# Performance work log

Hardware: AMD Instinct MI355X
Metric: run time of the kernel (lower is better)

## Reference

```python
import jax, jax.numpy as jnp
import numpy as np


def setup_inputs() -> dict:
    key = jax.random.key(0)
    ks = jax.random.split(key, 4)
    B, T, D, H = 64, 512, 512, 1024
    return {
        "x": jax.random.normal(ks[0], (B, T, D), dtype=jnp.float32),
        "kz": jax.random.normal(ks[1], (D, H), dtype=jnp.float32) * (1.0 / np.sqrt(D)),
        "kr": jax.random.normal(ks[2], (D, H), dtype=jnp.float32) * (1.0 / np.sqrt(D)),
        "kh": jax.random.normal(ks[3], (D, H), dtype=jnp.float32) * (1.0 / np.sqrt(D)),
        "mz": jnp.ones((H,), dtype=jnp.float32),
        "mr": jnp.ones((H,), dtype=jnp.float32),
        "br": jnp.zeros((H,), dtype=jnp.float32),
        "bz": jnp.zeros((H,), dtype=jnp.float32),
    }


def reference(x, kz, kr, kh, mz, mr, br, bz):
    B, T, D = x.shape
    H = kz.shape[1]
    # Precompute input projections for all timesteps (batched GEMMs),
    # identical math to per-step matmuls in the original cell.
    xz = jnp.einsum("btd,dh->bth", x, kz)  # [B,T,H]
    xr = jnp.einsum("btd,dh->bth", x, kr)
    xh = jnp.einsum("btd,dh->bth", x, kh)

    def step(h, inp):
        xz_t, xr_t, xh_t = inp  # each [B,H]
        r = jnp.tanh(xr_t + h * mr + br) + 1.0
        z = jax.nn.sigmoid(xz_t + h * mz + bz)
        h_new = z * h + (1.0 - z) * jnp.tanh(xh_t + r * h)
        return h_new, h_new

    h0 = jnp.zeros((B, H), dtype=x.dtype)
    # scan over time axis: move T to leading dim
    xs = (jnp.swapaxes(xz, 0, 1), jnp.swapaxes(xr, 0, 1), jnp.swapaxes(xh, 0, 1))
    _, ys = jax.lax.scan(step, h0, xs)  # ys: [T,B,H]
    return jnp.swapaxes(ys, 0, 1)  # [B,T,H]
```

## Files before the change

kernel.cpp:

```cpp
#include <hip/hip_runtime.h>
#include <hip/hip_bf16.h>
#include <math.h>


#define M_DIM 32768
#define K_DIM 512
#define H_DIM 1024
#define N3    3072

typedef _Float16 half8v __attribute__((ext_vector_type(8)));
typedef _Float16 half4v __attribute__((ext_vector_type(4)));
typedef float f32x4 __attribute__((ext_vector_type(4)));

__device__ __forceinline__ f32x4 mfma16(half8v a, half8v b, f32x4 c) {
    return __builtin_amdgcn_mfma_f32_16x16x32_f16(a, b, c, 0, 0, 0);
}

__device__ __forceinline__ void load_lds16(const void* g, void* l) {
    __builtin_amdgcn_global_load_lds(
        (const __attribute__((address_space(1))) void*)g,
        (__attribute__((address_space(3))) void*)l, 16, 0, 0);
}

__global__ __launch_bounds__(256) void convert_x(
    const float4* __restrict__ x4, half4v* __restrict__ hi4,
    half4v* __restrict__ lo4, int n4)
{
    int i = blockIdx.x * 256 + threadIdx.x;
    if (i >= n4) return;
    float4 v = x4[i];
    half4v h, lo;
    h.x = (_Float16)v.x; lo.x = (_Float16)(v.x - (float)h.x);
    h.y = (_Float16)v.y; lo.y = (_Float16)(v.y - (float)h.y);
    h.z = (_Float16)v.z; lo.z = (_Float16)(v.z - (float)h.z);
    h.w = (_Float16)v.w; lo.w = (_Float16)(v.w - (float)h.w);
    hi4[i] = h; lo4[i] = lo;
}

__global__ __launch_bounds__(256) void convert_wt_t(
    const float* __restrict__ kz, const float* __restrict__ kr,
    const float* __restrict__ kh, _Float16* __restrict__ wth,
    _Float16* __restrict__ wtl)
{
    __shared__ float lds[64][65];
    const int bid = blockIdx.x;
    const int w = bid >> 7;
    const int rem = bid & 127;
    const int k0 = (rem >> 4) * 64;
    const int n0 = (rem & 15) * 64;
    const int tid = threadIdx.x;
    const float* s = (w == 0) ? kz : ((w == 1) ? kr : kh);

#pragma unroll
    for (int r = 0; r < 4; ++r) {
        const int kk = (tid >> 4) + r * 16;
        const int nn = (tid & 15) * 4;
        float4 v = *(const float4*)&s[(size_t)(k0 + kk) * H_DIM + n0 + nn];
        lds[kk][nn + 0] = v.x; lds[kk][nn + 1] = v.y;
        lds[kk][nn + 2] = v.z; lds[kk][nn + 3] = v.w;
    }
    __syncthreads();
#pragma unroll
    for (int r = 0; r < 4; ++r) {
        const int nr = (tid >> 4) + r * 16;
        const int kb = (tid & 15) * 4;
        half4v hi, lo;
#pragma unroll
        for (int i = 0; i < 4; ++i) {
            float v = lds[kb + i][nr];
            _Float16 h = (_Float16)v;
            hi[i] = h; lo[i] = (_Float16)(v - (float)h);
        }
        const size_t o = ((size_t)(w * H_DIM + n0 + nr)) * K_DIM + k0 + kb;
        *(half4v*)&wth[o] = hi;
        *(half4v*)&wtl[o] = lo;
    }
}

template<bool TR>
__global__ __launch_bounds__(256) void gemm_mfma_split(
    const _Float16* __restrict__ Ahi, const _Float16* __restrict__ Alo,
    const _Float16* __restrict__ Bthi, const _Float16* __restrict__ Btlo,
    float* __restrict__ XZ, float* __restrict__ XR, float* __restrict__ OUT)
{
    __shared__ _Float16 Ah[128 * 32];
    __shared__ _Float16 Al[128 * 32];
    __shared__ _Float16 Bh[128 * 32];
    __shared__ _Float16 Bl[128 * 32];

    const int tid = threadIdx.x;
    const int w = tid >> 6, l = tid & 63;
    const int l15 = l & 15, quad = l >> 4;
    const int bx = blockIdx.x, by = blockIdx.y;
    const long m0 = (long)by * 128;
    const long n0 = (long)bx * 128;

    f32x4 acc[4][4] = {};

    const int s1 = tid, s2 = tid + 256;
    const long aoff1 = (m0 + (s1 >> 2)) * K_DIM + (s1 & 3) * 8;
    const long aoff2 = (m0 + (s2 >> 2)) * K_DIM + (s2 & 3) * 8;
    const long boff1 = (n0 + (s1 >> 2)) * K_DIM + (s1 & 3) * 8;
    const long boff2 = (n0 + (s2 >> 2)) * K_DIM + (s2 & 3) * 8;

    const _Float16* a1 = Ahi + aoff1;  const _Float16* a2 = Ahi + aoff2;
    const _Float16* q1 = Alo + aoff1;  const _Float16* q2 = Alo + aoff2;
    const _Float16* b1 = Bthi + boff1; const _Float16* b2 = Bthi + boff2;
    const _Float16* c1 = Btlo + boff1; const _Float16* c2 = Btlo + boff2;

    _Float16* ldsA1 = &Ah[w * 512]; _Float16* ldsA2 = &Ah[2048 + w * 512];
    _Float16* ldsQ1 = &Al[w * 512]; _Float16* ldsQ2 = &Al[2048 + w * 512];
    _Float16* ldsB1 = &Bh[w * 512]; _Float16* ldsB2 = &Bh[2048 + w * 512];
    _Float16* ldsC1 = &Bl[w * 512]; _Float16* ldsC2 = &Bl[2048 + w * 512];

    const int wm = (w >> 1) * 64, wn = (w & 1) * 64;

    for (int kk = 0; kk < K_DIM / 32; ++kk) {
        load_lds16(a1, ldsA1); load_lds16(a2, ldsA2);
        load_lds16(q1, ldsQ1); load_lds16(q2, ldsQ2);
        load_lds16(b1, ldsB1); load_lds16(b2, ldsB2);
        load_lds16(c1, ldsC1); load_lds16(c2, ldsC2);
        a1 += 32; a2 += 32; q1 += 32; q2 += 32;
        b1 += 32; b2 += 32; c1 += 32; c2 += 32;
        __syncthreads();

        half8v afh[4], afl[4], bfh[4], bfl[4];
#pragma unroll
        for (int mi = 0; mi < 4; ++mi) {
            int row = (wm + mi * 16 + l15) * 32 + quad * 8;
            afh[mi] = *(const half8v*)&Ah[row];
            afl[mi] = *(const half8v*)&Al[row];
        }
#pragma unroll
        for (int ni = 0; ni < 4; ++ni) {
            int row = (wn + ni * 16 + l15) * 32 + quad * 8;
            bfh[ni] = *(const half8v*)&Bh[row];
            bfl[ni] = *(const half8v*)&Bl[row];
        }
#pragma unroll
        for (int mi = 0; mi < 4; ++mi)
#pragma unroll
            for (int ni = 0; ni < 4; ++ni) {
                acc[mi][ni] = mfma16(afh[mi], bfh[ni], acc[mi][ni]);
                acc[mi][ni] = mfma16(afh[mi], bfl[ni], acc[mi][ni]);
                acc[mi][ni] = mfma16(afl[mi], bfh[ni], acc[mi][ni]);
            }
        __syncthreads();
    }

    if (!TR) {
        float* dst = (bx < 8) ? XZ : ((bx < 16) ? XR : OUT);
        const long nl = (long)(bx & 7) * 128 + wn + l15;
#pragma unroll
        for (int mi = 0; mi < 4; ++mi) {
            const long m = m0 + wm + mi * 16 + quad * 4;
#pragma unroll
            for (int ni = 0; ni < 4; ++ni) {
                float* p = dst + m * H_DIM + nl + ni * 16;
#pragma unroll
                for (int i = 0; i < 4; ++i)
                    p[(long)i * H_DIM] = acc[mi][ni][i];
            }
        }
    } else {
        float* dst = (bx < 8) ? XZ : ((bx < 16) ? XR : OUT);
#pragma unroll
        for (int mi = 0; mi < 4; ++mi) {
            const long m = m0 + wm + mi * 16 + quad * 4;
            const long b = m >> 9;
            const long t = m & 511;
#pragma unroll
            for (int ni = 0; ni < 4; ++ni) {
                const long n = (long)(bx & 7) * 128 + wn + ni * 16 + l15;
                *(f32x4*)&dst[((size_t)(b * H_DIM + n) << 9) + t] = acc[mi][ni];
            }
        }
    }
}

#define BM 128
#define BN 128
#define BK 8
__global__ __launch_bounds__(256) void gemm_f32(
    const float* __restrict__ A, const float* __restrict__ B,
    float* __restrict__ C, int M, int N, int K)
{
    __shared__ float As[BK][BM];
    __shared__ float Bs[BK][BN];
    const int tid = threadIdx.x;
    const int bm = blockIdx.y * BM, bn = blockIdx.x * BN;
    const int tx = tid & 15, ty = tid >> 4;
    float acc[8][8];
#pragma unroll
    for (int i = 0; i < 8; i++)
#pragma unroll
        for (int j = 0; j < 8; j++) acc[i][j] = 0.f;
    const int a_row = tid >> 1, a_k = (tid & 1) * 4;
    const int b_row = tid >> 5, b_col = (tid & 31) * 4;
    const float* Aptr = A + (size_t)(bm + a_row) * K + a_k;
    const float* Bptr = B + (size_t)b_row * N + bn + b_col;
    for (int k0 = 0; k0 < K; k0 += BK) {
        float4 av = *(const float4*)(Aptr + k0);
        float4 bv = *(const float4*)(Bptr + (size_t)k0 * N);
        As[a_k + 0][a_row] = av.x; As[a_k + 1][a_row] = av.y;
        As[a_k + 2][a_row] = av.z; As[a_k + 3][a_row] = av.w;
        *(float4*)&Bs[b_row][b_col] = bv;
        __syncthreads();
#pragma unroll
        for (int kk = 0; kk < BK; kk++) {
            float4 a0 = *(const float4*)&As[kk][ty * 8];
            float4 a1 = *(const float4*)&As[kk][ty * 8 + 4];
            float4 b0 = *(const float4*)&Bs[kk][tx * 8];
            float4 b1 = *(const float4*)&Bs[kk][tx * 8 + 4];
            float a[8] = {a0.x, a0.y, a0.z, a0.w, a1.x, a1.y, a1.z, a1.w};
            float b[8] = {b0.x, b0.y, b0.z, b0.w, b1.x, b1.y, b1.z, b1.w};
#pragma unroll
            for (int i = 0; i < 8; i++)
#pragma unroll
                for (int j = 0; j < 8; j++)
                    acc[i][j] = fmaf(a[i], b[j], acc[i][j]);
        }
        __syncthreads();
    }
    float* Cptr = C + (size_t)(bm + ty * 8) * N + bn + tx * 8;
#pragma unroll
    for (int i = 0; i < 8; i++) {
        float4 c0 = {acc[i][0], acc[i][1], acc[i][2], acc[i][3]};
        float4 c1 = {acc[i][4], acc[i][5], acc[i][6], acc[i][7]};
        *(float4*)(Cptr + (size_t)i * N)     = c0;
        *(float4*)(Cptr + (size_t)i * N + 4) = c1;
    }
}

__device__ __forceinline__ float vrcp_nr(float d) {
    float r = __builtin_amdgcn_rcpf(d);
    return r * fmaf(-d, r, 2.0f);
}

__global__ __launch_bounds__(256) void scan_t(
    const float* __restrict__ XZt, const float* __restrict__ XRt,
    const float* __restrict__ XHt, float* __restrict__ out,
    const float* __restrict__ mz, const float* __restrict__ mr,
    const float* __restrict__ br, const float* __restrict__ bz)
{
    const int gid = blockIdx.x * blockDim.x + threadIdx.x;
    const int b = gid >> 10;
    const int h = gid & (H_DIM - 1);

    const float mzK = -mz[h];
    const float mrK = -2.0f * mr[h];
    const float bzK = -bz[h];
    const float brK = -2.0f * br[h];
    float hs = 0.f;

    const size_t sbase = ((size_t)(b * H_DIM + h)) << 9;
    const float4* pz = (const float4*)(XZt + sbase);
    const float4* pr = (const float4*)(XRt + sbase);
    const float4* ph = (const float4*)(XHt + sbase);
    float* const po = out + ((size_t)b << 19) + h;

    float cz[32], cr[32], ch[32];
#pragma unroll
    for (int q = 0; q < 8; ++q) {
        float4 vz = pz[q], vr = pr[q], vh = ph[q];
        cz[q*4+0] = bzK - vz.x; cz[q*4+1] = bzK - vz.y;
        cz[q*4+2] = bzK - vz.z; cz[q*4+3] = bzK - vz.w;
        cr[q*4+0] = fmaf(-2.0f, vr.x, brK); cr[q*4+1] = fmaf(-2.0f, vr.y, brK);
        cr[q*4+2] = fmaf(-2.0f, vr.z, brK); cr[q*4+3] = fmaf(-2.0f, vr.w, brK);
        ch[q*4+0] = -2.0f * vh.x; ch[q*4+1] = -2.0f * vh.y;
        ch[q*4+2] = -2.0f * vh.z; ch[q*4+3] = -2.0f * vh.w;
    }
    for (int t0 = 0; t0 < 512; t0 += 32) {
        float4 nz4[8], nr4[8], nh4[8];
        const bool more = (t0 + 32) < 512;
        if (more) {
            const int b4 = (t0 + 32) >> 2;
#pragma unroll
            for (int q = 0; q < 8; ++q) {
                nz4[q] = pz[b4 + q]; nr4[q] = pr[b4 + q]; nh4[q] = ph[b4 + q];
            }
        }
        float* pout = po + ((size_t)t0 << 10);
#pragma unroll
        for (int j = 0; j < 32; ++j) {
            const float u1   = fmaf(hs, mrK, cr[j]);
            const float uz   = fmaf(hs, mzK, cz[j]);
            const float hsK2 = -4.0f * hs;
            const float e1 = __expf(u1);
            const float s1 = vrcp_nr(e1 + 1.0f);
            const float ez = __expf(uz);
            const float sz = vrcp_nr(ez + 1.0f);
            const float u2 = fmaf(s1, hsK2, ch[j]);
            const float e2 = __expf(u2);
            const float s2 = vrcp_nr(e2 + 1.0f);
            const float th = fmaf(2.0f, s2, -1.0f);
            const float hn = fmaf(sz, hs - th, th);
            *pout = hn; pout += H_DIM;
            hs = hn;
        }
        if (more) {
#pragma unroll
            for (int q = 0; q < 8; ++q) {
                cz[q*4+0] = bzK - nz4[q].x; cz[q*4+1] = bzK - nz4[q].y;
                cz[q*4+2] = bzK - nz4[q].z; cz[q*4+3] = bzK - nz4[q].w;
                cr[q*4+0] = fmaf(-2.0f, nr4[q].x, brK);
                cr[q*4+1] = fmaf(-2.0f, nr4[q].y, brK);
                cr[q*4+2] = fmaf(-2.0f, nr4[q].z, brK);
                cr[q*4+3] = fmaf(-2.0f, nr4[q].w, brK);
                ch[q*4+0] = -2.0f * nh4[q].x; ch[q*4+1] = -2.0f * nh4[q].y;
                ch[q*4+2] = -2.0f * nh4[q].z; ch[q*4+3] = -2.0f * nh4[q].w;
            }
        }
    }
}

__global__ __launch_bounds__(256) void scan_kernel(
    const float* __restrict__ XZ, const float* __restrict__ XR,
    float* __restrict__ OUT,
    const float* __restrict__ mz, const float* __restrict__ mr,
    const float* __restrict__ br, const float* __restrict__ bz)
{
    const int gid = blockIdx.x * blockDim.x + threadIdx.x;
    const int b = gid >> 10;
    const int h = gid & (H_DIM - 1);

    const float mzK = -mz[h];
    const float mrK = -2.0f * mr[h];
    const float bzK = -bz[h];
    const float brK = -2.0f * br[h];
    float hs = 0.f;
    size_t idx = (size_t)b * 512 * H_DIM + h;

    float cz[16], cr[16], ch[16];
#pragma unroll
    for (int j = 0; j < 16; ++j) {
        cz[j] = bzK - XZ[idx + (size_t)j * H_DIM];
        cr[j] = fmaf(-2.0f, XR[idx + (size_t)j * H_DIM], brK);
        ch[j] = -2.0f * OUT[idx + (size_t)j * H_DIM];
    }
    for (int t0 = 0; t0 < 512; t0 += 16) {
        float nz[16], nr[16], nh[16];
        const bool more = (t0 + 16) < 512;
        const size_t nidx = idx + 16ul * H_DIM;
        if (more) {
#pragma unroll
            for (int j = 0; j < 16; ++j) {
                nz[j] = XZ[nidx + (size_t)j * H_DIM];
                nr[j] = XR[nidx + (size_t)j * H_DIM];
                nh[j] = OUT[nidx + (size_t)j * H_DIM];
            }
        }
#pragma unroll
        for (int j = 0; j < 16; ++j) {
            const float u1   = fmaf(hs, mrK, cr[j]);
            const float uz   = fmaf(hs, mzK, cz[j]);
            const float hsK2 = -4.0f * hs;
            const float e1 = __expf(u1);
            const float s1 = vrcp_nr(e1 + 1.0f);
            const float ez = __expf(uz);
            const float sz = vrcp_nr(ez + 1.0f);
            const float u2 = fmaf(s1, hsK2, ch[j]);
            const float e2 = __expf(u2);
            const float s2 = vrcp_nr(e2 + 1.0f);
            const float th = fmaf(2.0f, s2, -1.0f);
            const float hn = fmaf(sz, hs - th, th);
            OUT[idx + (size_t)j * H_DIM] = hn;
            hs = hn;
        }
        idx = nidx;
        if (more) {
#pragma unroll
            for (int j = 0; j < 16; ++j) {
                cz[j] = bzK - nz[j];
                cr[j] = fmaf(-2.0f, nr[j], brK);
                ch[j] = -2.0f * nh[j];
            }
        }
    }
}

extern "C" void kernel_launch(void* const* d_in, const int* in_sizes, int n_in,
                              void* d_out, int out_size, void* d_ws, size_t ws_size,
                              hipStream_t stream) {
    const float* x  = (const float*)d_in[0];
    const float* kz = (const float*)d_in[1];
    const float* kr = (const float*)d_in[2];
    const float* kh = (const float*)d_in[3];
    const float* mz = (const float*)d_in[4];
    const float* mr = (const float*)d_in[5];
    const float* br = (const float*)d_in[6];
    const float* bz = (const float*)d_in[7];
    float* out = (float*)d_out;

    char* ws = (char*)d_ws;
    const int n4 = M_DIM * K_DIM / 4;

    const size_t need_t = 476053504ul;
    const size_t need_o = 341835776ul;

    if (ws_size >= need_t) {
        float* XZt = (float*)ws;
        float* XRt = (float*)(ws + 134217728ul);
        float* XHt = (float*)(ws + 268435456ul);
        _Float16* XHI = (_Float16*)(ws + 402653184ul);
        _Float16* XLO = (_Float16*)(ws + 436207616ul);
        _Float16* WTH = (_Float16*)(ws + 469762048ul);
        _Float16* WTL = (_Float16*)(ws + 472907776ul);

        convert_x<<<n4 / 256, 256, 0, stream>>>(
            (const float4*)x, (half4v*)XHI, (half4v*)XLO, n4);
        convert_wt_t<<<384, 256, 0, stream>>>(kz, kr, kh, WTH, WTL);
        dim3 grid(N3 / 128, M_DIM / 128);
        gemm_mfma_split<true><<<grid, 256, 0, stream>>>(
            XHI, XLO, WTH, WTL, XZt, XRt, XHt);
        scan_t<<<(64 * H_DIM) / 256, 256, 0, stream>>>(
            XZt, XRt, XHt, out, mz, mr, br, bz);
    } else if (ws_size >= need_o) {
        float* XZ = (float*)ws;
        float* XR = (float*)(ws + 134217728ul);
        _Float16* XHI = (_Float16*)(ws + 268435456ul);
        _Float16* XLO = (_Float16*)(ws + 301989888ul);
        _Float16* WTH = (_Float16*)(ws + 335544320ul);
        _Float16* WTL = (_Float16*)(ws + 338690048ul);

        convert_x<<<n4 / 256, 256, 0, stream>>>(
            (const float4*)x, (half4v*)XHI, (half4v*)XLO, n4);
        convert_wt_t<<<384, 256, 0, stream>>>(kz, kr, kh, WTH, WTL);
        dim3 grid(N3 / 128, M_DIM / 128);
        gemm_mfma_split<false><<<grid, 256, 0, stream>>>(
            XHI, XLO, WTH, WTL, XZ, XR, out);
        scan_kernel<<<(64 * H_DIM) / 256, 256, 0, stream>>>(
            XZ, XR, out, mz, mr, br, bz);
    } else {
        float* XZ = (float*)ws;
        float* XR = (float*)(ws + 134217728ul);
        dim3 grid(H_DIM / BN, M_DIM / BM);
        gemm_f32<<<grid, 256, 0, stream>>>(x, kz, XZ,  M_DIM, H_DIM, K_DIM);
        gemm_f32<<<grid, 256, 0, stream>>>(x, kr, XR,  M_DIM, H_DIM, K_DIM);
        gemm_f32<<<grid, 256, 0, stream>>>(x, kh, out, M_DIM, H_DIM, K_DIM);
        scan_kernel<<<(64 * H_DIM) / 256, 256, 0, stream>>>(
            XZ, XR, out, mz, mr, br, bz);
    }
}
```

Measured before the change: 601.6 us.

## Store GEMM projections row-major with padded stride instead of transposed layout

The GEMM epilogue now writes XZ/XR/XH in [B*T, H] layout with a padded row stride of 1088 instead of the per-(b,h) time-contiguous transposed layout. The scan reads one coalesced element per thread per timestep across h, prefetching 16 steps ahead instead of 32. The padding is meant to avoid channel/bank conflicts from power-of-two strides, and the coalesced reads replace per-thread float4 loads strided by 2KB. It uses more workspace and has scalar strided reads and a shorter prefetch window.

```diff
diff --git a/kernel.cpp b/kernel.cpp
--- a/kernel.cpp
+++ b/kernel.cpp
@@ -6,6 +6,7 @@
 #define M_DIM 32768
 #define K_DIM 512
 #define H_DIM 1024
+#define HPAD  1088
 #define N3    3072
 
 typedef _Float16 half8v __attribute__((ext_vector_type(8)));
@@ -77,7 +78,7 @@
     }
 }
 
-template<bool TR>
+template<bool PAD>
 __global__ __launch_bounds__(256) void gemm_mfma_split(
     const _Float16* __restrict__ Ahi, const _Float16* __restrict__ Alo,
     const _Float16* __restrict__ Bthi, const _Float16* __restrict__ Btlo,
@@ -148,32 +149,18 @@
         __syncthreads();
     }
 
-    if (!TR) {
-        float* dst = (bx < 8) ? XZ : ((bx < 16) ? XR : OUT);
-        const long nl = (long)(bx & 7) * 128 + wn + l15;
-#pragma unroll
-        for (int mi = 0; mi < 4; ++mi) {
-            const long m = m0 + wm + mi * 16 + quad * 4;
-#pragma unroll
-            for (int ni = 0; ni < 4; ++ni) {
-                float* p = dst + m * H_DIM + nl + ni * 16;
-#pragma unroll
-                for (int i = 0; i < 4; ++i)
-                    p[(long)i * H_DIM] = acc[mi][ni][i];
-            }
-        }
-    } else {
-        float* dst = (bx < 8) ? XZ : ((bx < 16) ? XR : OUT);
-#pragma unroll
-        for (int mi = 0; mi < 4; ++mi) {
-            const long m = m0 + wm + mi * 16 + quad * 4;
-            const long b = m >> 9;
-            const long t = m & 511;
-#pragma unroll
-            for (int ni = 0; ni < 4; ++ni) {
-                const long n = (long)(bx & 7) * 128 + wn + ni * 16 + l15;
-                *(f32x4*)&dst[((size_t)(b * H_DIM + n) << 9) + t] = acc[mi][ni];
-            }
+    const long stride = PAD ? HPAD : H_DIM;
+    float* dst = (bx < 8) ? XZ : ((bx < 16) ? XR : OUT);
+    const long nl = (long)(bx & 7) * 128 + wn + l15;
+#pragma unroll
+    for (int mi = 0; mi < 4; ++mi) {
+        const long m = m0 + wm + mi * 16 + quad * 4;
+#pragma unroll
+        for (int ni = 0; ni < 4; ++ni) {
+            float* p = dst + m * stride + nl + ni * 16;
+#pragma unroll
+            for (int i = 0; i < 4; ++i)
+                p[(long)i * stride] = acc[mi][ni][i];
         }
     }
 }
@@ -237,9 +224,9 @@
     return r * fmaf(-d, r, 2.0f);
 }
 
-__global__ __launch_bounds__(256) void scan_t(
-    const float* __restrict__ XZt, const float* __restrict__ XRt,
-    const float* __restrict__ XHt, float* __restrict__ out,
+__global__ __launch_bounds__(256) void scan_pad(
+    const float* __restrict__ XZ, const float* __restrict__ XR,
+    const float* __restrict__ XH, float* __restrict__ out,
     const float* __restrict__ mz, const float* __restrict__ mr,
     const float* __restrict__ br, const float* __restrict__ bz)
 {
@@ -252,37 +239,30 @@
     const float bzK = -bz[h];
     const float brK = -2.0f * br[h];
     float hs = 0.f;
-
-    const size_t sbase = ((size_t)(b * H_DIM + h)) << 9;
-    const float4* pz = (const float4*)(XZt + sbase);
-    const float4* pr = (const float4*)(XRt + sbase);
-    const float4* ph = (const float4*)(XHt + sbase);
-    float* const po = out + ((size_t)b << 19) + h;
-
-    float cz[32], cr[32], ch[32];
-#pragma unroll
-    for (int q = 0; q < 8; ++q) {
-        float4 vz = pz[q], vr = pr[q], vh = ph[q];
-        cz[q*4+0] = bzK - vz.x; cz[q*4+1] = bzK - vz.y;
-        cz[q*4+2] = bzK - vz.z; cz[q*4+3] = bzK - vz.w;
-        cr[q*4+0] = fmaf(-2.0f, vr.x, brK); cr[q*4+1] = fmaf(-2.0f, vr.y, brK);
-        cr[q*4+2] = fmaf(-2.0f, vr.z, brK); cr[q*4+3] = fmaf(-2.0f, vr.w, brK);
-        ch[q*4+0] = -2.0f * vh.x; ch[q*4+1] = -2.0f * vh.y;
-        ch[q*4+2] = -2.0f * vh.z; ch[q*4+3] = -2.0f * vh.w;
-    }
-    for (int t0 = 0; t0 < 512; t0 += 32) {
-        float4 nz4[8], nr4[8], nh4[8];
-        const bool more = (t0 + 32) < 512;
+    size_t ri = (size_t)b * 512 * HPAD + h;
+    size_t wi = (size_t)b * 512 * H_DIM + h;
+
+    float cz[16], cr[16], ch[16];
+#pragma unroll
+    for (int j = 0; j < 16; ++j) {
+        cz[j] = bzK - XZ[ri + (size_t)j * HPAD];
+        cr[j] = fmaf(-2.0f, XR[ri + (size_t)j * HPAD], brK);
+        ch[j] = -2.0f * XH[ri + (size_t)j * HPAD];
+    }
+    for (int t0 = 0; t0 < 512; t0 += 16) {
+        float nz[16], nr[16], nh[16];
+        const bool more = (t0 + 16) < 512;
+        const size_t nri = ri + 16ul * HPAD;
         if (more) {
-            const int b4 = (t0 + 32) >> 2;
-#pragma unroll
-            for (int q = 0; q < 8; ++q) {
-                nz4[q] = pz[b4 + q]; nr4[q] = pr[b4 + q]; nh4[q] = ph[b4 + q];
+#pragma unroll
+            for (int j = 0; j < 16; ++j) {
+                nz[j] = XZ[nri + (size_t)j * HPAD];
+                nr[j] = XR[nri + (size_t)j * HPAD];
+                nh[j] = XH[nri + (size_t)j * HPAD];
             }
         }
-        float* pout = po + ((size_t)t0 << 10);
-#pragma unroll
-        for (int j = 0; j < 32; ++j) {
+#pragma unroll
+        for (int j = 0; j < 16; ++j) {
             const float u1   = fmaf(hs, mrK, cr[j]);
             const float uz   = fmaf(hs, mzK, cz[j]);
             const float hsK2 = -4.0f * hs;
@@ -295,20 +275,17 @@
             const float s2 = vrcp_nr(e2 + 1.0f);
             const float th = fmaf(2.0f, s2, -1.0f);
             const float hn = fmaf(sz, hs - th, th);
-            *pout = hn; pout += H_DIM;
+            out[wi + (size_t)j * H_DIM] = hn;
             hs = hn;
         }
+        ri = nri;
+        wi += 16ul * H_DIM;
         if (more) {
 #pragma unroll
-            for (int q = 0; q < 8; ++q) {
-                cz[q*4+0] = bzK - nz4[q].x; cz[q*4+1] = bzK - nz4[q].y;
-                cz[q*4+2] = bzK - nz4[q].z; cz[q*4+3] = bzK - nz4[q].w;
-                cr[q*4+0] = fmaf(-2.0f, nr4[q].x, brK);
-                cr[q*4+1] = fmaf(-2.0f, nr4[q].y, brK);
-                cr[q*4+2] = fmaf(-2.0f, nr4[q].z, brK);
-                cr[q*4+3] = fmaf(-2.0f, nr4[q].w, brK);
-                ch[q*4+0] = -2.0f * nh4[q].x; ch[q*4+1] = -2.0f * nh4[q].y;
-                ch[q*4+2] = -2.0f * nh4[q].z; ch[q*4+3] = -2.0f * nh4[q].w;
+            for (int j = 0; j < 16; ++j) {
+                cz[j] = bzK - nz[j];
+                cr[j] = fmaf(-2.0f, nr[j], brK);
+                ch[j] = -2.0f * nh[j];
             }
         }
     }
@@ -395,26 +372,27 @@
     char* ws = (char*)d_ws;
     const int n4 = M_DIM * K_DIM / 4;
 
-    const size_t need_t = 476053504ul;
-    const size_t need_o = 341835776ul;
-
-    if (ws_size >= need_t) {
-        float* XZt = (float*)ws;
-        float* XRt = (float*)(ws + 134217728ul);
-        float* XHt = (float*)(ws + 268435456ul);
-        _Float16* XHI = (_Float16*)(ws + 402653184ul);
-        _Float16* XLO = (_Float16*)(ws + 436207616ul);
-        _Float16* WTH = (_Float16*)(ws + 469762048ul);
-        _Float16* WTL = (_Float16*)(ws + 472907776ul);
+    const size_t PARR = (size_t)M_DIM * HPAD * 4ul;
+    const size_t need_pad = 3ul * PARR + 67108864ul + 6291456ul;
+    const size_t need_o   = 341835776ul;
+
+    if (ws_size >= need_pad) {
+        float* XZ = (float*)ws;
+        float* XR = (float*)(ws + PARR);
+        float* XH = (float*)(ws + 2 * PARR);
+        _Float16* XHI = (_Float16*)(ws + 3 * PARR);
+        _Float16* XLO = (_Float16*)(ws + 3 * PARR + 33554432ul);
+        _Float16* WTH = (_Float16*)(ws + 3 * PARR + 67108864ul);
+        _Float16* WTL = (_Float16*)(ws + 3 * PARR + 70254592ul);
 
         convert_x<<<n4 / 256, 256, 0, stream>>>(
             (const float4*)x, (half4v*)XHI, (half4v*)XLO, n4);
         convert_wt_t<<<384, 256, 0, stream>>>(kz, kr, kh, WTH, WTL);
         dim3 grid(N3 / 128, M_DIM / 128);
         gemm_mfma_split<true><<<grid, 256, 0, stream>>>(
-            XHI, XLO, WTH, WTL, XZt, XRt, XHt);
-        scan_t<<<(64 * H_DIM) / 256, 256, 0, stream>>>(
-            XZt, XRt, XHt, out, mz, mr, br, bz);
+            XHI, XLO, WTH, WTL, XZ, XR, XH);
+        scan_pad<<<(64 * H_DIM) / 256, 256, 0, stream>>>(
+            XZ, XR, XH, out, mz, mr, br, bz);
     } else if (ws_size >= need_o) {
         float* XZ = (float*)ws;
         float* XR = (float*)(ws + 134217728ul);
```

New measurement: 587.3 us. -2.4%, faster.
